# Performance work log

Hardware: AMD Instinct MI355X
Metric: run time of the kernel (lower is better)

## Reference

```python
import jax, jax.numpy as jnp
import numpy as np

C, G = 512, 16            # channels, groups
GC = C // G               # group channels = 32
OFFSET_SCALE = 1.0
EPS = 1e-6


def setup_inputs() -> dict:
    key = jax.random.key(0)
    ks = jax.random.split(key, 4)
    N, H, W = 8, 64, 64
    return {
        "input_first": jax.random.normal(ks[0], (N, C, H, W), jnp.float32),
        "input_last": jax.random.normal(ks[1], (N, H, W, C), jnp.float32),
        "dw_w": jax.random.normal(ks[2], (C, 1, 3, 3), jnp.float32) * 0.1,  # depthwise kernel (OIHW, I=1)
        "dw_b": jnp.zeros((C,), jnp.float32),
        "ln_g": jnp.ones((C,), jnp.float32),
        "ln_b": jnp.zeros((C,), jnp.float32),
        "off_w": jax.random.normal(ks[3], (2 * G, C), jnp.float32) * 0.02,  # nonzero (module zero-inits)
        "off_b": jnp.zeros((2 * G,), jnp.float32),
    }


def _bilinear(img, px, py):
    # align_corners=False, padding_mode='zeros'.
    Hin, Win, _ = img.shape
    x0 = jnp.floor(px)
    y0 = jnp.floor(py)
    wx1 = px - x0
    wy1 = py - y0

    def tap(xi, yi, w):
        xc = jnp.clip(xi, 0, Win - 1).astype(jnp.int32)
        yc = jnp.clip(yi, 0, Hin - 1).astype(jnp.int32)
        valid = ((xi >= 0) & (xi <= Win - 1) & (yi >= 0) & (yi <= Hin - 1)).astype(img.dtype)
        return img[yc, xc] * (w * valid)[:, None]  # [L, GC]

    return (tap(x0, y0, (1 - wx1) * (1 - wy1)) + tap(x0 + 1, y0, wx1 * (1 - wy1)) +
            tap(x0, y0 + 1, (1 - wx1) * wy1) + tap(x0 + 1, y0 + 1, wx1 * wy1))


_sampler = jax.vmap(jax.vmap(_bilinear))  # over [N, G, ...]


def _forward(input_first, input_last, dw_w, dw_b, ln_g, ln_b, off_w, off_b):
    N, _, H, W = input_first.shape
    # --- dw_conv: depthwise 3x3 conv (pad 1) -> LN (channels_last) -> GELU ---
    x = jax.lax.conv_general_dilated(
        input_first, dw_w, window_strides=(1, 1), padding='SAME',
        dimension_numbers=('NCHW', 'OIHW', 'NCHW'), feature_group_count=C)
    x = x + dw_b[None, :, None, None]
    x = jnp.transpose(x, (0, 2, 3, 1))  # NHWC
    mu = x.mean(-1, keepdims=True)
    var = x.var(-1, keepdims=True)
    x1 = (x - mu) * jax.lax.rsqrt(var + EPS) * ln_g + ln_b
    x1 = jax.nn.gelu(x1, approximate=False)

    # --- offset prediction: [N,H,W, G*2], pairs are (x, y) per DCNv3 layout ---
    off = jnp.einsum('nhwc,oc->nhwo', x1, off_w) + off_b
    off = off.reshape(N, H, W, G, 2)

    # --- DCNv3 core, kernel_size=1, pad=0, stride=1, dilation=1 ---
    # ref point = pixel center; normalized loc = (i+0.5)/size + off*scale/size;
    # grid_sample pixel coord = loc*size - 0.5 = i + off*scale.
    px = jnp.arange(W, dtype=x1.dtype)[None, None, :, None] + off[..., 0] * OFFSET_SCALE  # [N,H,W,G]
    py = jnp.arange(H, dtype=x1.dtype)[None, :, None, None] + off[..., 1] * OFFSET_SCALE
    px = px.transpose(0, 3, 1, 2).reshape(N, G, H * W)
    py = py.transpose(0, 3, 1, 2).reshape(N, G, H * W)

    img = input_last.reshape(N, H, W, G, GC).transpose(0, 3, 1, 2, 4)  # [N,G,H,W,GC]
    sampled = _sampler(img, px, py)  # [N,G,HW,GC]

    mask = jnp.ones((N, G, H * W, 1), dtype=input_last.dtype)  # mask_dcn = ones
    out = (sampled * mask).reshape(N, G, H, W, GC)
    out = out.transpose(0, 2, 3, 1, 4).reshape(N, H, W, C)
    return jnp.transpose(out, (0, 3, 1, 2))  # NCHW, as in module's final permute


def reference(input_first, input_last, dw_w, dw_b, ln_g, ln_b, off_w, off_b):
    return _forward(input_first, input_last, dw_w, dw_b, ln_g, ln_b, off_w, off_b)
```

## Files before the change

### kernel.cpp

```cpp
#include <hip/hip_runtime.h>
#include <hip/hip_bf16.h>
#include <math.h>

#define NB 8
#define CC 512
#define HH 64
#define WW 64
#define GG 16
#define GCH 32
#define OO 32
#define NGHW (NB * GG * HH * WW)
#define NPX  (NB * HH * WW)
#define XROW 520


__device__ __forceinline__ float gelu_exact(float x) {
    return 0.5f * x * (1.0f + erff(x * 0.70710678118654752f));
}

__device__ __forceinline__ unsigned pack_bf2(float a, float b) {
    __hip_bfloat162 t = __float22bfloat162_rn(make_float2(a, b));
    return *(unsigned*)&t;
}

typedef __attribute__((ext_vector_type(8))) short bf16x8;
typedef __attribute__((ext_vector_type(4))) float f32x4;

__global__ __launch_bounds__(1024, 4)
void fused_conv_ln_gelu_off_kernel(const float* __restrict__ in_first,
                                   const float* __restrict__ dw_w,
                                   const float* __restrict__ dw_b,
                                   const float* __restrict__ ln_g,
                                   const float* __restrict__ ln_b,
                                   const float* __restrict__ off_w,
                                   const float* __restrict__ off_b,
                                   float* __restrict__ coords)
{
    const int h    = blockIdx.x;
    const int n    = blockIdx.y;
    const int tid  = threadIdx.x;
    const int wq   = tid & 31;
    const int cgrp = tid >> 5;
    const int wb   = wq * 2;
    const int c0   = cgrp * 16;
    const int wave = tid >> 6;
    const int lane = tid & 63;

    __shared__ short xbuf[64 * XROW];
    __shared__ float redS [16 * 64];
    __shared__ float redS2[16 * 64];
    __shared__ float mu_s[64];
    __shared__ float rs_s[64];

    float xv[2][16];
    float sw0 = 0.f, sw1 = 0.f, sq0 = 0.f, sq1 = 0.f;

    const float* inbase = in_first + (size_t)(n * CC + c0) * HH * WW;

    #pragma unroll
    for (int i = 0; i < 16; ++i) {
        const int c = c0 + i;
        float w9[9];
        #pragma unroll
        for (int k = 0; k < 9; ++k) w9[k] = dw_w[c * 9 + k];
        const float b = dw_b[c];
        float a0 = b, a1 = b;
        #pragma unroll
        for (int r = 0; r < 3; ++r) {
            const int y = h + r - 1;
            if (y < 0 || y >= HH) continue;
            const float2 m = *(const float2*)(inbase + ((size_t)i * HH + y) * WW + wb);
            float left  = __shfl_up(m.y, 1);
            float right = __shfl_down(m.x, 1);
            if (wq == 0)  left  = 0.0f;
            if (wq == 31) right = 0.0f;
            const float k0 = w9[r * 3 + 0], k1 = w9[r * 3 + 1], k2 = w9[r * 3 + 2];
            a0 += k0 * left + k1 * m.x + k2 * m.y;
            a1 += k0 * m.x  + k1 * m.y + k2 * right;
        }
        xv[0][i] = a0; xv[1][i] = a1;
        sw0 += a0; sq0 += a0 * a0;
        sw1 += a1; sq1 += a1 * a1;
    }

    sw0 += __shfl_xor(sw0, 32); sq0 += __shfl_xor(sq0, 32);
    sw1 += __shfl_xor(sw1, 32); sq1 += __shfl_xor(sq1, 32);
    if (lane < 32) {
        redS [wave * 64 + wb + 0] = sw0;  redS2[wave * 64 + wb + 0] = sq0;
        redS [wave * 64 + wb + 1] = sw1;  redS2[wave * 64 + wb + 1] = sq1;
    }
    __syncthreads();
    if (tid < 64) {
        float s = 0.f, s2 = 0.f;
        #pragma unroll
        for (int k = 0; k < 16; ++k) {
            s  += redS [k * 64 + tid];
            s2 += redS2[k * 64 + tid];
        }
        const float mu  = s * (1.0f / 512.0f);
        const float var = s2 * (1.0f / 512.0f) - mu * mu;
        mu_s[tid] = mu;
        rs_s[tid] = rsqrtf(var + 1e-6f);
    }
    __syncthreads();

    {
        const float mu0 = mu_s[wb + 0], rs0 = rs_s[wb + 0];
        const float mu1 = mu_s[wb + 1], rs1 = rs_s[wb + 1];
        unsigned pk0[8], pk1[8];
        #pragma unroll
        for (int t = 0; t < 8; ++t) {
            const int c = c0 + 2 * t;
            const float lgA = ln_g[c],     lbA = ln_b[c];
            const float lgB = ln_g[c + 1], lbB = ln_b[c + 1];
            const float v0a = (xv[0][2 * t]     - mu0) * rs0 * lgA + lbA;
            const float v0b = (xv[0][2 * t + 1] - mu0) * rs0 * lgB + lbB;
            const float v1a = (xv[1][2 * t]     - mu1) * rs1 * lgA + lbA;
            const float v1b = (xv[1][2 * t + 1] - mu1) * rs1 * lgB + lbB;
            pk0[t] = pack_bf2(gelu_exact(v0a), gelu_exact(v0b));
            pk1[t] = pack_bf2(gelu_exact(v1a), gelu_exact(v1b));
        }
        short* p0 = xbuf + (wb + 0) * XROW + c0;
        short* p1 = xbuf + (wb + 1) * XROW + c0;
        *(uint4*)(p0)     = make_uint4(pk0[0], pk0[1], pk0[2], pk0[3]);
        *(uint4*)(p0 + 8) = make_uint4(pk0[4], pk0[5], pk0[6], pk0[7]);
        *(uint4*)(p1)     = make_uint4(pk1[0], pk1[1], pk1[2], pk1[3]);
        *(uint4*)(p1 + 8) = make_uint4(pk1[4], pk1[5], pk1[6], pk1[7]);
    }
    __syncthreads();

    if (wave < 8) {
        const int ml   = lane & 15;
        const int quad = lane >> 4;
        const int pxT  = wave >> 1;
        const int oT   = wave & 1;

        const short* arow = xbuf + (pxT * 16 + ml) * XROW + quad * 8;
        const float* brow = off_w + (size_t)(oT * 16 + ml) * CC + quad * 8;

        f32x4 acc = {0.f, 0.f, 0.f, 0.f};
        for (int k = 0; k < CC; k += 32) {
            const bf16x8 af = *(const bf16x8*)(arow + k);
            const float4 p = *(const float4*)(brow + k);
            const float4 q = *(const float4*)(brow + k + 4);
            union { bf16x8 v; unsigned u[4]; } bb;
            bb.u[0] = pack_bf2(p.x, p.y); bb.u[1] = pack_bf2(p.z, p.w);
            bb.u[2] = pack_bf2(q.x, q.y); bb.u[3] = pack_bf2(q.z, q.w);
            acc = __builtin_amdgcn_mfma_f32_16x16x32_bf16(af, bb.v, acc, 0, 0, 0);
        }

        const int   o   = oT * 16 + ml;
        const float ob  = off_b[o];
        const int   par = o & 1;
        const int   g   = o >> 1;
        #pragma unroll
        for (int r = 0; r < 4; ++r) {
            const int w = pxT * 16 + quad * 4 + r;
            const float base = par ? (float)h : (float)w;
            coords[(size_t)par * NGHW + (((size_t)n * GG + g) * HH + h) * WW + w]
                = base + acc[r] + ob;
        }
    }
}

__global__ __launch_bounds__(256)
void sample_kernel(const float* __restrict__ in_last,
                   const float* __restrict__ coord_ws,
                   float* __restrict__ out)
{
    const int h   = blockIdx.x;
    const int n   = blockIdx.y;
    const int g   = blockIdx.z;
    const int tid = threadIdx.x;

    __shared__ float pxs[64];
    __shared__ float pys[64];
    __shared__ float smem[64 * 33];

    if (tid < 128) {
        const int w = tid & 63;
        const size_t cidx = (((size_t)n * GG + g) * HH + h) * WW + w;
        if (tid < 64) pxs[w] = coord_ws[cidx];
        else          pys[w] = coord_ws[cidx + NGHW];
    }
    __syncthreads();

    const int c4    = tid & 7;
    const int wslot = tid >> 3;
    const float* base = in_last + (size_t)n * HH * WW * CC + g * GCH + c4 * 4;

    #pragma unroll
    for (int pass = 0; pass < 2; ++pass) {
        const int w = wslot + pass * 32;
        const float px = pxs[w];
        const float py = pys[w];
        const float x0f = floorf(px), y0f = floorf(py);
        const float fx = px - x0f, fy = py - y0f;
        const int x0 = (int)x0f, y0 = (int)y0f;

        float4 acc = make_float4(0.f, 0.f, 0.f, 0.f);
        #pragma unroll
        for (int t = 0; t < 4; ++t) {
            const int xi = x0 + (t & 1);
            const int yi = y0 + (t >> 1);
            const float wt = ((t & 1) ? fx : 1.0f - fx) * ((t >> 1) ? fy : 1.0f - fy);
            if (xi >= 0 && xi < WW && yi >= 0 && yi < HH) {
                const float4 v = *(const float4*)(base + ((size_t)yi * WW + xi) * CC);
                acc.x += wt * v.x;
                acc.y += wt * v.y;
                acc.z += wt * v.z;
                acc.w += wt * v.w;
            }
        }
        float* sp = smem + w * 33 + c4 * 4;
        sp[0] = acc.x; sp[1] = acc.y; sp[2] = acc.z; sp[3] = acc.w;
    }
    __syncthreads();

    const int w  = tid & 63;
    const int cb = tid >> 6;
    float* op = out + (((size_t)n * CC + g * GCH) * HH + h) * WW + w;
    #pragma unroll
    for (int pass = 0; pass < 8; ++pass) {
        const int c = pass * 4 + cb;
        op[(size_t)c * (HH * WW)] = smem[w * 33 + c];
    }
}

extern "C" void kernel_launch(void* const* d_in, const int* in_sizes, int n_in,
                              void* d_out, int out_size, void* d_ws, size_t ws_size,
                              hipStream_t stream) {
    const float* in_first = (const float*)d_in[0];
    const float* in_last  = (const float*)d_in[1];
    const float* dw_w     = (const float*)d_in[2];
    const float* dw_b     = (const float*)d_in[3];
    const float* ln_g     = (const float*)d_in[4];
    const float* ln_b     = (const float*)d_in[5];
    const float* off_w    = (const float*)d_in[6];
    const float* off_b    = (const float*)d_in[7];
    float* out = (float*)d_out;

    float* coord_ws = (float*)d_ws;

    dim3 gridA(HH, NB);
    fused_conv_ln_gelu_off_kernel<<<gridA, 1024, 0, stream>>>(
        in_first, dw_w, dw_b, ln_g, ln_b, off_w, off_b, coord_ws);

    dim3 gridB(HH, NB, GG);
    sample_kernel<<<gridB, 256, 0, stream>>>(in_last, coord_ws, out);
}
```

Measured before the change: 282.7 us.

## Widen conv loads, alias reduction buffers, batch sampler gathers, remap blocks, vectorize stores

In the fused conv/LN/offset kernel each thread now handles 4 pixels by 8 channels with float4 loads instead of 2 by 16 with float2. The reduction scratch arrays are aliased into xbuf to cut LDS use, and the launch bound now requests 8 blocks per CU. In the sampler, all eight bilinear gathers are issued up front with clamped addresses and zeroed weights, so the loads overlap instead of sitting behind branches. Blocks are remapped with a stride-8 swizzle, presumably to spread work across XCDs, and output stores are widened to float4. The risks are more register pressure and possible LDS bank conflicts on the transposed reads.

```diff
diff --git a/kernel.cpp b/kernel.cpp
--- a/kernel.cpp
+++ b/kernel.cpp
@@ -26,7 +26,7 @@
 typedef __attribute__((ext_vector_type(8))) short bf16x8;
 typedef __attribute__((ext_vector_type(4))) float f32x4;
 
-__global__ __launch_bounds__(1024, 4)
+__global__ __launch_bounds__(1024, 8)
 void fused_conv_ln_gelu_off_kernel(const float* __restrict__ in_first,
                                    const float* __restrict__ dw_w,
                                    const float* __restrict__ dw_b,
@@ -39,55 +39,66 @@
     const int h    = blockIdx.x;
     const int n    = blockIdx.y;
     const int tid  = threadIdx.x;
-    const int wq   = tid & 31;
-    const int cgrp = tid >> 5;
-    const int wb   = wq * 2;
-    const int c0   = cgrp * 16;
+    const int wq   = tid & 15;
+    const int cgrp = tid >> 4;
+    const int wb   = wq * 4;
+    const int c0   = cgrp * 8;
     const int wave = tid >> 6;
     const int lane = tid & 63;
 
     __shared__ short xbuf[64 * XROW];
-    __shared__ float redS [16 * 64];
-    __shared__ float redS2[16 * 64];
     __shared__ float mu_s[64];
     __shared__ float rs_s[64];
-
-    float xv[2][16];
-    float sw0 = 0.f, sw1 = 0.f, sq0 = 0.f, sq1 = 0.f;
-
-    const float* inbase = in_first + (size_t)(n * CC + c0) * HH * WW;
-
-    #pragma unroll
-    for (int i = 0; i < 16; ++i) {
+    float* redS  = (float*)xbuf;
+    float* redS2 = (float*)xbuf + 1024;
+
+    float xv[4][8];
+    float sw[4] = {0.f, 0.f, 0.f, 0.f};
+    float sq[4] = {0.f, 0.f, 0.f, 0.f};
+
+    const float* inbase = in_first + ((size_t)n * CC + c0) * HH * WW;
+
+    #pragma unroll
+    for (int i = 0; i < 8; ++i) {
         const int c = c0 + i;
         float w9[9];
         #pragma unroll
         for (int k = 0; k < 9; ++k) w9[k] = dw_w[c * 9 + k];
         const float b = dw_b[c];
-        float a0 = b, a1 = b;
+        float a0 = b, a1 = b, a2 = b, a3 = b;
         #pragma unroll
         for (int r = 0; r < 3; ++r) {
             const int y = h + r - 1;
             if (y < 0 || y >= HH) continue;
-            const float2 m = *(const float2*)(inbase + ((size_t)i * HH + y) * WW + wb);
-            float left  = __shfl_up(m.y, 1);
+            const float4 m = *(const float4*)(inbase + ((size_t)i * HH + y) * WW + wb);
+            float left  = __shfl_up(m.w, 1);
             float right = __shfl_down(m.x, 1);
             if (wq == 0)  left  = 0.0f;
-            if (wq == 31) right = 0.0f;
+            if (wq == 15) right = 0.0f;
             const float k0 = w9[r * 3 + 0], k1 = w9[r * 3 + 1], k2 = w9[r * 3 + 2];
             a0 += k0 * left + k1 * m.x + k2 * m.y;
-            a1 += k0 * m.x  + k1 * m.y + k2 * right;
-        }
-        xv[0][i] = a0; xv[1][i] = a1;
-        sw0 += a0; sq0 += a0 * a0;
-        sw1 += a1; sq1 += a1 * a1;
-    }
-
-    sw0 += __shfl_xor(sw0, 32); sq0 += __shfl_xor(sq0, 32);
-    sw1 += __shfl_xor(sw1, 32); sq1 += __shfl_xor(sq1, 32);
-    if (lane < 32) {
-        redS [wave * 64 + wb + 0] = sw0;  redS2[wave * 64 + wb + 0] = sq0;
-        redS [wave * 64 + wb + 1] = sw1;  redS2[wave * 64 + wb + 1] = sq1;
+            a1 += k0 * m.x  + k1 * m.y + k2 * m.z;
+            a2 += k0 * m.y  + k1 * m.z + k2 * m.w;
+            a3 += k0 * m.z  + k1 * m.w + k2 * right;
+        }
+        xv[0][i] = a0; xv[1][i] = a1; xv[2][i] = a2; xv[3][i] = a3;
+        sw[0] += a0; sq[0] += a0 * a0;
+        sw[1] += a1; sq[1] += a1 * a1;
+        sw[2] += a2; sq[2] += a2 * a2;
+        sw[3] += a3; sq[3] += a3 * a3;
+    }
+
+    #pragma unroll
+    for (int j = 0; j < 4; ++j) {
+        sw[j] += __shfl_xor(sw[j], 16); sw[j] += __shfl_xor(sw[j], 32);
+        sq[j] += __shfl_xor(sq[j], 16); sq[j] += __shfl_xor(sq[j], 32);
+    }
+    if (lane < 16) {
+        #pragma unroll
+        for (int j = 0; j < 4; ++j) {
+            redS [wave * 64 + wb + j] = sw[j];
+            redS2[wave * 64 + wb + j] = sq[j];
+        }
     }
     __syncthreads();
     if (tid < 64) {
@@ -105,27 +116,27 @@
     __syncthreads();
 
     {
-        const float mu0 = mu_s[wb + 0], rs0 = rs_s[wb + 0];
-        const float mu1 = mu_s[wb + 1], rs1 = rs_s[wb + 1];
-        unsigned pk0[8], pk1[8];
-        #pragma unroll
-        for (int t = 0; t < 8; ++t) {
+        float mu_[4], rs_[4];
+        #pragma unroll
+        for (int j = 0; j < 4; ++j) { mu_[j] = mu_s[wb + j]; rs_[j] = rs_s[wb + j]; }
+        unsigned pk[4][4];
+        #pragma unroll
+        for (int t = 0; t < 4; ++t) {
             const int c = c0 + 2 * t;
             const float lgA = ln_g[c],     lbA = ln_b[c];
             const float lgB = ln_g[c + 1], lbB = ln_b[c + 1];
-            const float v0a = (xv[0][2 * t]     - mu0) * rs0 * lgA + lbA;
-            const float v0b = (xv[0][2 * t + 1] - mu0) * rs0 * lgB + lbB;
-            const float v1a = (xv[1][2 * t]     - mu1) * rs1 * lgA + lbA;
-            const float v1b = (xv[1][2 * t + 1] - mu1) * rs1 * lgB + lbB;
-            pk0[t] = pack_bf2(gelu_exact(v0a), gelu_exact(v0b));
-            pk1[t] = pack_bf2(gelu_exact(v1a), gelu_exact(v1b));
-        }
-        short* p0 = xbuf + (wb + 0) * XROW + c0;
-        short* p1 = xbuf + (wb + 1) * XROW + c0;
-        *(uint4*)(p0)     = make_uint4(pk0[0], pk0[1], pk0[2], pk0[3]);
-        *(uint4*)(p0 + 8) = make_uint4(pk0[4], pk0[5], pk0[6], pk0[7]);
-        *(uint4*)(p1)     = make_uint4(pk1[0], pk1[1], pk1[2], pk1[3]);
-        *(uint4*)(p1 + 8) = make_uint4(pk1[4], pk1[5], pk1[6], pk1[7]);
+            #pragma unroll
+            for (int j = 0; j < 4; ++j) {
+                const float va = (xv[j][2 * t]     - mu_[j]) * rs_[j] * lgA + lbA;
+                const float vb = (xv[j][2 * t + 1] - mu_[j]) * rs_[j] * lgB + lbB;
+                pk[j][t] = pack_bf2(gelu_exact(va), gelu_exact(vb));
+            }
+        }
+        #pragma unroll
+        for (int j = 0; j < 4; ++j) {
+            *(uint4*)(xbuf + (size_t)(wb + j) * XROW + c0)
+                = make_uint4(pk[j][0], pk[j][1], pk[j][2], pk[j][3]);
+        }
     }
     __syncthreads();
 
@@ -135,7 +146,7 @@
         const int pxT  = wave >> 1;
         const int oT   = wave & 1;
 
-        const short* arow = xbuf + (pxT * 16 + ml) * XROW + quad * 8;
+        const short* arow = xbuf + (size_t)(pxT * 16 + ml) * XROW + quad * 8;
         const float* brow = off_w + (size_t)(oT * 16 + ml) * CC + quad * 8;
 
         f32x4 acc = {0.f, 0.f, 0.f, 0.f};
@@ -168,9 +179,11 @@
                    const float* __restrict__ coord_ws,
                    float* __restrict__ out)
 {
-    const int h   = blockIdx.x;
-    const int n   = blockIdx.y;
-    const int g   = blockIdx.z;
+    const int bid = blockIdx.x;
+    const int nb  = (bid & 7) * 1024 + (bid >> 3);
+    const int h   = nb & 63;
+    const int n   = (nb >> 6) & 7;
+    const int g   = nb >> 9;
     const int tid = threadIdx.x;
 
     __shared__ float pxs[64];
@@ -189,41 +202,59 @@
     const int wslot = tid >> 3;
     const float* base = in_last + (size_t)n * HH * WW * CC + g * GCH + c4 * 4;
 
-    #pragma unroll
-    for (int pass = 0; pass < 2; ++pass) {
-        const int w = wslot + pass * 32;
+    int   off[8];
+    float wt [8];
+    #pragma unroll
+    for (int p = 0; p < 2; ++p) {
+        const int w = wslot + p * 32;
         const float px = pxs[w];
         const float py = pys[w];
         const float x0f = floorf(px), y0f = floorf(py);
         const float fx = px - x0f, fy = py - y0f;
         const int x0 = (int)x0f, y0 = (int)y0f;
-
-        float4 acc = make_float4(0.f, 0.f, 0.f, 0.f);
         #pragma unroll
         for (int t = 0; t < 4; ++t) {
             const int xi = x0 + (t & 1);
             const int yi = y0 + (t >> 1);
-            const float wt = ((t & 1) ? fx : 1.0f - fx) * ((t >> 1) ? fy : 1.0f - fy);
-            if (xi >= 0 && xi < WW && yi >= 0 && yi < HH) {
-                const float4 v = *(const float4*)(base + ((size_t)yi * WW + xi) * CC);
-                acc.x += wt * v.x;
-                acc.y += wt * v.y;
-                acc.z += wt * v.z;
-                acc.w += wt * v.w;
-            }
-        }
-        float* sp = smem + w * 33 + c4 * 4;
-        sp[0] = acc.x; sp[1] = acc.y; sp[2] = acc.z; sp[3] = acc.w;
-    }
-    __syncthreads();
-
-    const int w  = tid & 63;
-    const int cb = tid >> 6;
-    float* op = out + (((size_t)n * CC + g * GCH) * HH + h) * WW + w;
-    #pragma unroll
-    for (int pass = 0; pass < 8; ++pass) {
-        const int c = pass * 4 + cb;
-        op[(size_t)c * (HH * WW)] = smem[w * 33 + c];
+            const int xc = min(max(xi, 0), WW - 1);
+            const int yc = min(max(yi, 0), HH - 1);
+            const float valid = (xi >= 0 && xi < WW && yi >= 0 && yi < HH) ? 1.0f : 0.0f;
+            wt [p * 4 + t] = ((t & 1) ? fx : 1.0f - fx) * ((t >> 1) ? fy : 1.0f - fy) * valid;
+            off[p * 4 + t] = (yc * WW + xc) * CC;
+        }
+    }
+    float4 v[8];
+    #pragma unroll
+    for (int i = 0; i < 8; ++i) v[i] = *(const float4*)(base + off[i]);
+
+    float4 a0 = make_float4(0.f, 0.f, 0.f, 0.f);
+    float4 a1 = make_float4(0.f, 0.f, 0.f, 0.f);
+    #pragma unroll
+    for (int t = 0; t < 4; ++t) {
+        a0.x += wt[t] * v[t].x;     a0.y += wt[t] * v[t].y;
+        a0.z += wt[t] * v[t].z;     a0.w += wt[t] * v[t].w;
+        a1.x += wt[4 + t] * v[4 + t].x; a1.y += wt[4 + t] * v[4 + t].y;
+        a1.z += wt[4 + t] * v[4 + t].z; a1.w += wt[4 + t] * v[4 + t].w;
+    }
+    {
+        float* sp0 = smem + wslot * 33 + c4 * 4;
+        float* sp1 = smem + (wslot + 32) * 33 + c4 * 4;
+        sp0[0] = a0.x; sp0[1] = a0.y; sp0[2] = a0.z; sp0[3] = a0.w;
+        sp1[0] = a1.x; sp1[1] = a1.y; sp1[2] = a1.z; sp1[3] = a1.w;
+    }
+    __syncthreads();
+
+    const int c  = tid >> 4;
+    const int w4 = (tid & 15) * 4;
+    #pragma unroll
+    for (int p = 0; p < 2; ++p) {
+        const int cc = c + p * 16;
+        float4 o;
+        o.x = smem[(w4 + 0) * 33 + cc];
+        o.y = smem[(w4 + 1) * 33 + cc];
+        o.z = smem[(w4 + 2) * 33 + cc];
+        o.w = smem[(w4 + 3) * 33 + cc];
+        *(float4*)(out + (((size_t)n * CC + g * GCH + cc) * HH + h) * WW + w4) = o;
     }
 }
 
@@ -246,6 +277,5 @@
     fused_conv_ln_gelu_off_kernel<<<gridA, 1024, 0, stream>>>(
         in_first, dw_w, dw_b, ln_g, ln_b, off_w, off_b, coord_ws);
 
-    dim3 gridB(HH, NB, GG);
-    sample_kernel<<<gridB, 256, 0, stream>>>(in_last, coord_ws, out);
-}
+    sample_kernel<<<HH * NB * GG, 256, 0, stream>>>(in_last, coord_ws, out);
+}
```

Result: faster. 247.3 us (-12.6%).
